# Kernel optimization log

Hardware: AMD Instinct MI355X
Metric: run time of the kernel (lower is better)

Reference implementation:

```python
import jax, jax.numpy as jnp
import numpy as np

N_NODES = 50000
NEG_SLOPE = 0.2


def setup_inputs() -> dict:
    key = jax.random.key(0)
    k1, k2, k3, k4 = jax.random.split(key, 4)
    N, E, F, H, C = 50000, 800000, 128, 4, 32
    x = jax.random.normal(k1, (N, F), dtype=jnp.float32)
    edge_index = jax.random.randint(k2, (2, E), 0, N, dtype=jnp.int32)
    weight = jax.random.normal(k3, (F, H * C), dtype=jnp.float32) * 0.1  # glorot-ish scale
    att = jax.random.normal(k4, (1, H, 2 * C), dtype=jnp.float32) * 0.1
    bias = jnp.zeros((C,), dtype=jnp.float32)
    return {"x": x, "edge_index": edge_index, "weight": weight, "att": att, "bias": bias}


def reference(x, edge_index, weight, att, bias):
    N = x.shape[0]
    H, C2 = att.shape[1], att.shape[2]
    C = C2 // 2
    # linear projection -> [N, H, C]
    xw = jnp.matmul(x, weight).reshape(N, H, C)
    row, col = edge_index[0], edge_index[1]
    # per-edge attention logits: gather both endpoints, concat along channel
    x_i = xw[row]                     # [E, H, C]
    x_j = xw[col]                     # [E, H, C]
    cat_x = jnp.concatenate([x_i, x_j], axis=-1)      # [E, H, 2C]
    alpha = jnp.sum(cat_x * att, axis=-1)             # [E, H]
    alpha = jnp.where(alpha >= 0, alpha, NEG_SLOPE * alpha)  # leaky_relu
    # segment softmax grouped by row (source index, as in the torch code)
    seg_max = jax.ops.segment_max(alpha, row, num_segments=N)
    seg_max = jnp.where(jnp.isfinite(seg_max), seg_max, 0.0)
    alpha = jnp.exp(alpha - seg_max[row])
    seg_sum = jax.ops.segment_sum(alpha, row, num_segments=N)
    alpha = alpha / (seg_sum[row] + 1e-16)            # [E, H]
    # PyG propagate: message = alpha * x_j where x_j = x[edge_index[0]],
    # aggregated (scatter-add) into target = edge_index[1]
    msg = alpha[..., None] * xw[row]                  # [E, H, C]
    out = jax.ops.segment_sum(msg, col, num_segments=N)  # [N, H, C]
    out = out.mean(axis=1) + bias                     # concat=False -> head mean, + bias
    return out
```

## Files before the change

### kernel.cpp

```cpp
#include <hip/hip_runtime.h>
#include <hip/hip_fp16.h>

#define FDIM 128
#define HEADS 4
#define CD 32
#define BM 64
#define XPAD 68

static __device__ __forceinline__ unsigned short f2bf(float v) {
    unsigned u = __float_as_uint(v);
    u += 0x7FFF + ((u >> 16) & 1);
    return (unsigned short)(u >> 16);
}
static __device__ __forceinline__ float bf2f(unsigned short u) {
    return __uint_as_float(((unsigned)u) << 16);
}

__global__ __launch_bounds__(256) void k_gemm(const float* __restrict__ x,
                                              const float* __restrict__ w,
                                              unsigned short* __restrict__ xwh,
                                              float4* __restrict__ zero_base,
                                              int nz4, int N)
{
    __shared__ float xs[FDIM * XPAD];
    int t = threadIdx.x;
    int row0 = blockIdx.x * BM;
    for (int i = blockIdx.x * 256 + t; i < nz4; i += gridDim.x * 256)
        zero_base[i] = make_float4(0.f, 0.f, 0.f, 0.f);
#pragma unroll
    for (int it = 0; it < 8; it++) {
        int i = t + 256 * it;
        int row = i & 63, kq = i >> 6;
        float4 v = make_float4(0.f, 0.f, 0.f, 0.f);
        if (row0 + row < N) v = ((const float4*)x)[(size_t)(row0 + row) * 32 + kq];
        xs[(kq * 4 + 0) * XPAD + row] = v.x;
        xs[(kq * 4 + 1) * XPAD + row] = v.y;
        xs[(kq * 4 + 2) * XPAD + row] = v.z;
        xs[(kq * 4 + 3) * XPAD + row] = v.w;
    }
    __syncthreads();
    int tx = t & 31, ty = t >> 5;
    int c0 = tx * 4, r0 = ty * 8;
    const float4* w4 = (const float4*)w;
    float acc[8][4];
#pragma unroll
    for (int i = 0; i < 8; i++)
#pragma unroll
        for (int j = 0; j < 4; j++) acc[i][j] = 0.f;
#pragma unroll 4
    for (int k = 0; k < FDIM; k++) {
        float4 wv = w4[k * 32 + tx];
        float4 xa = *(const float4*)&xs[k * XPAD + r0];
        float4 xb = *(const float4*)&xs[k * XPAD + r0 + 4];
        float xr[8] = {xa.x, xa.y, xa.z, xa.w, xb.x, xb.y, xb.z, xb.w};
        float wr[4] = {wv.x, wv.y, wv.z, wv.w};
#pragma unroll
        for (int i = 0; i < 8; i++)
#pragma unroll
            for (int j = 0; j < 4; j++) acc[i][j] += xr[i] * wr[j];
    }
    int h = c0 >> 5, chb = c0 & 31;
#pragma unroll
    for (int i = 0; i < 8; i++) {
        int r = row0 + r0 + i;
        if (r < N) {
#pragma unroll
            for (int j = 0; j < 4; j++)
                xwh[(size_t)r * FDIM + (chb + j) * 4 + h] = f2bf(acc[i][j]);
        }
    }
}

__global__ __launch_bounds__(256) void k_logits(const unsigned short* __restrict__ xwh,
                                                const float* __restrict__ att,
                                                float* __restrict__ a_src,
                                                float* __restrict__ a_dst, int N)
{
    __shared__ float attl[HEADS * 2 * CD];
    int t = threadIdx.x;
    attl[t] = att[t];
    __syncthreads();
    int n = blockIdx.x * 256 + t;
    if (n >= N) return;
    const ushort4* xp = (const ushort4*)(xwh + (size_t)n * FDIM);
    float s[4] = {0.f, 0.f, 0.f, 0.f}, d[4] = {0.f, 0.f, 0.f, 0.f};
#pragma unroll 8
    for (int c = 0; c < CD; c++) {
        ushort4 p = xp[c];
        float f0 = bf2f(p.x), f1 = bf2f(p.y), f2 = bf2f(p.z), f3 = bf2f(p.w);
        s[0] += f0 * attl[0 * 64 + c];  d[0] += f0 * attl[0 * 64 + 32 + c];
        s[1] += f1 * attl[1 * 64 + c];  d[1] += f1 * attl[1 * 64 + 32 + c];
        s[2] += f2 * attl[2 * 64 + c];  d[2] += f2 * attl[2 * 64 + 32 + c];
        s[3] += f3 * attl[3 * 64 + c];  d[3] += f3 * attl[3 * 64 + 32 + c];
    }
    *(float4*)&a_src[n * 4] = make_float4(s[0], s[1], s[2], s[3]);
    *(float4*)&a_dst[n * 4] = make_float4(d[0], d[1], d[2], d[3]);
}

__global__ __launch_bounds__(256) void k_esum(const int* __restrict__ ei, int E,
                                              const float* __restrict__ a_src,
                                              const float* __restrict__ a_dst,
                                              float* __restrict__ seg,
                                              float* __restrict__ ealpha)
{
    int gid = blockIdx.x * 256 + threadIdx.x;
    if (gid >= E * HEADS) return;
    int e = gid >> 2, h = gid & 3;
    int r = ei[e], cl = ei[E + e];
    float a = a_src[r * 4 + h] + a_dst[cl * 4 + h];
    a = a >= 0.f ? a : 0.2f * a;
    float ex = __expf(a);
    ealpha[gid] = ex;
    atomicAdd(&seg[r * 4 + h], ex);
}

__global__ __launch_bounds__(256) void k_scatter(const int* __restrict__ ei, int E,
                                                 const float* __restrict__ ealpha,
                                                 const float* __restrict__ seg,
                                                 const unsigned short* __restrict__ xwh,
                                                 __half2* __restrict__ out_acc2)
{
    int t = threadIdx.x;
    int le = t >> 4, c2 = t & 15;
    int e = blockIdx.x * 16 + le;
    if (e >= E) return;
    int r = ei[e], cl = ei[E + e];
    int lane = t & 63;
    float av = 0.f;
    if (c2 < 4) av = 0.25f * ealpha[e * 4 + c2] / (seg[r * 4 + c2] + 1e-16f);
    uint4 q = ((const uint4*)(xwh + (size_t)r * FDIM))[c2];
    float a0 = __shfl(av, (lane & 48) + 0, 64);
    float a1 = __shfl(av, (lane & 48) + 1, 64);
    float a2 = __shfl(av, (lane & 48) + 2, 64);
    float a3 = __shfl(av, (lane & 48) + 3, 64);
    float v0 = a0 * bf2f((unsigned short)(q.x & 0xFFFF)) + a1 * bf2f((unsigned short)(q.x >> 16))
             + a2 * bf2f((unsigned short)(q.y & 0xFFFF)) + a3 * bf2f((unsigned short)(q.y >> 16));
    float v1 = a0 * bf2f((unsigned short)(q.z & 0xFFFF)) + a1 * bf2f((unsigned short)(q.z >> 16))
             + a2 * bf2f((unsigned short)(q.w & 0xFFFF)) + a3 * bf2f((unsigned short)(q.w >> 16));
    unsafeAtomicAdd(&out_acc2[(size_t)cl * 16 + c2], __floats2half2_rn(v0, v1));
}

__global__ void k_final(const __half2* __restrict__ out_acc2, const float4* __restrict__ bias,
                        float4* __restrict__ out, int N)
{
    int i = blockIdx.x * 256 + threadIdx.x;
    if (i >= N * 8) return;
    float4 b = bias[i & 7];
    float2 f0 = __half22float2(out_acc2[i * 2]);
    float2 f1 = __half22float2(out_acc2[i * 2 + 1]);
    out[i] = make_float4(f0.x + b.x, f0.y + b.y, f1.x + b.z, f1.y + b.w);
}

extern "C" void kernel_launch(void* const* d_in, const int* in_sizes, int n_in,
                              void* d_out, int out_size, void* d_ws, size_t ws_size,
                              hipStream_t stream)
{
    const float* x    = (const float*)d_in[0];
    const int*   ei   = (const int*)d_in[1];
    const float* w    = (const float*)d_in[2];
    const float* att  = (const float*)d_in[3];
    const float* bias = (const float*)d_in[4];
    float* out = (float*)d_out;
    int N = in_sizes[0] / FDIM;
    int E = in_sizes[1] / 2;

    unsigned short* xwh = (unsigned short*)d_ws;
    float* fws      = (float*)(xwh + (size_t)N * FDIM);
    float* a_src    = fws;
    float* a_dst    = a_src + (size_t)N * HEADS;
    float* ealpha   = a_dst + (size_t)N * HEADS;
    float* seg      = ealpha + (size_t)E * HEADS;
    __half2* out_acc2 = (__half2*)(seg + (size_t)N * HEADS);

    int nz4 = (N * HEADS + N * CD / 2 + 3) / 4;

    k_gemm<<<(N + BM - 1) / BM, 256, 0, stream>>>(x, w, xwh, (float4*)seg, nz4, N);
    k_logits<<<(N + 255) / 256, 256, 0, stream>>>(xwh, att, a_src, a_dst, N);
    k_esum<<<(E * HEADS + 255) / 256, 256, 0, stream>>>(ei, E, a_src, a_dst, seg, ealpha);
    k_scatter<<<(E + 15) / 16, 256, 0, stream>>>(ei, E, ealpha, seg, xwh, out_acc2);
    k_final<<<(N * 8 + 255) / 256, 256, 0, stream>>>(out_acc2, (const float4*)bias, (float4*)out, N);
}
```

Baseline: 214.1 us.

## Fuse attention logit computation into GEMM epilogue and store edge exps as fp16

The separate logits kernel is removed. After the GEMM, each block stages its fp32 accumulators in shared memory and computes the per-node source and destination attention dot products there, which saves a kernel launch and a re-read of the bf16 projection. The per-edge exponentials are now stored as half precision instead of float, halving that intermediate buffer's traffic between the edge-sum and scatter kernels. The logits now use fp32 values instead of bf16-rounded ones, which changes numerics slightly. The fp16 exps could overflow for large logits.

```diff
diff --git a/kernel.cpp b/kernel.cpp
--- a/kernel.cpp
+++ b/kernel.cpp
@@ -18,15 +18,20 @@
 
 __global__ __launch_bounds__(256) void k_gemm(const float* __restrict__ x,
                                               const float* __restrict__ w,
+                                              const float* __restrict__ att,
                                               unsigned short* __restrict__ xwh,
+                                              float* __restrict__ a_src,
+                                              float* __restrict__ a_dst,
                                               float4* __restrict__ zero_base,
                                               int nz4, int N)
 {
     __shared__ float xs[FDIM * XPAD];
+    __shared__ float attl[HEADS * 2 * CD];
     int t = threadIdx.x;
     int row0 = blockIdx.x * BM;
     for (int i = blockIdx.x * 256 + t; i < nz4; i += gridDim.x * 256)
         zero_base[i] = make_float4(0.f, 0.f, 0.f, 0.f);
+    attl[t] = att[t];
 #pragma unroll
     for (int it = 0; it < 8; it++) {
         int i = t + 256 * it;
@@ -59,49 +64,38 @@
 #pragma unroll
             for (int j = 0; j < 4; j++) acc[i][j] += xr[i] * wr[j];
     }
-    int h = c0 >> 5, chb = c0 & 31;
+    int h0 = c0 >> 5, chb = c0 & 31;
 #pragma unroll
     for (int i = 0; i < 8; i++) {
         int r = row0 + r0 + i;
         if (r < N) {
 #pragma unroll
             for (int j = 0; j < 4; j++)
-                xwh[(size_t)r * FDIM + (chb + j) * 4 + h] = f2bf(acc[i][j]);
+                xwh[(size_t)r * FDIM + (chb + j) * 4 + h0] = f2bf(acc[i][j]);
         }
     }
-}
-
-__global__ __launch_bounds__(256) void k_logits(const unsigned short* __restrict__ xwh,
-                                                const float* __restrict__ att,
-                                                float* __restrict__ a_src,
-                                                float* __restrict__ a_dst, int N)
-{
-    __shared__ float attl[HEADS * 2 * CD];
-    int t = threadIdx.x;
-    attl[t] = att[t];
     __syncthreads();
-    int n = blockIdx.x * 256 + t;
-    if (n >= N) return;
-    const ushort4* xp = (const ushort4*)(xwh + (size_t)n * FDIM);
-    float s[4] = {0.f, 0.f, 0.f, 0.f}, d[4] = {0.f, 0.f, 0.f, 0.f};
+    float* accs = xs;
+#pragma unroll
+    for (int i = 0; i < 8; i++)
+        *(float4*)&accs[(r0 + i) * 132 + c0] =
+            make_float4(acc[i][0], acc[i][1], acc[i][2], acc[i][3]);
+    __syncthreads();
+    int row = t >> 2, h = t & 3;
+    const float* ap = &attl[h * 2 * CD];
+    const float* xr = &accs[row * 132 + h * CD];
+    float s = 0.f, d = 0.f;
 #pragma unroll 8
-    for (int c = 0; c < CD; c++) {
-        ushort4 p = xp[c];
-        float f0 = bf2f(p.x), f1 = bf2f(p.y), f2 = bf2f(p.z), f3 = bf2f(p.w);
-        s[0] += f0 * attl[0 * 64 + c];  d[0] += f0 * attl[0 * 64 + 32 + c];
-        s[1] += f1 * attl[1 * 64 + c];  d[1] += f1 * attl[1 * 64 + 32 + c];
-        s[2] += f2 * attl[2 * 64 + c];  d[2] += f2 * attl[2 * 64 + 32 + c];
-        s[3] += f3 * attl[3 * 64 + c];  d[3] += f3 * attl[3 * 64 + 32 + c];
-    }
-    *(float4*)&a_src[n * 4] = make_float4(s[0], s[1], s[2], s[3]);
-    *(float4*)&a_dst[n * 4] = make_float4(d[0], d[1], d[2], d[3]);
+    for (int c = 0; c < CD; c++) { float v = xr[c]; s += v * ap[c]; d += v * ap[CD + c]; }
+    int n = row0 + row;
+    if (n < N) { a_src[n * 4 + h] = s; a_dst[n * 4 + h] = d; }
 }
 
 __global__ __launch_bounds__(256) void k_esum(const int* __restrict__ ei, int E,
                                               const float* __restrict__ a_src,
                                               const float* __restrict__ a_dst,
                                               float* __restrict__ seg,
-                                              float* __restrict__ ealpha)
+                                              __half* __restrict__ ealpha)
 {
     int gid = blockIdx.x * 256 + threadIdx.x;
     if (gid >= E * HEADS) return;
@@ -110,12 +104,12 @@
     float a = a_src[r * 4 + h] + a_dst[cl * 4 + h];
     a = a >= 0.f ? a : 0.2f * a;
     float ex = __expf(a);
-    ealpha[gid] = ex;
+    ealpha[gid] = __float2half(ex);
     atomicAdd(&seg[r * 4 + h], ex);
 }
 
 __global__ __launch_bounds__(256) void k_scatter(const int* __restrict__ ei, int E,
-                                                 const float* __restrict__ ealpha,
+                                                 const __half* __restrict__ ealpha,
                                                  const float* __restrict__ seg,
                                                  const unsigned short* __restrict__ xwh,
                                                  __half2* __restrict__ out_acc2)
@@ -127,7 +121,7 @@
     int r = ei[e], cl = ei[E + e];
     int lane = t & 63;
     float av = 0.f;
-    if (c2 < 4) av = 0.25f * ealpha[e * 4 + c2] / (seg[r * 4 + c2] + 1e-16f);
+    if (c2 < 4) av = 0.25f * __half2float(ealpha[e * 4 + c2]) / (seg[r * 4 + c2] + 1e-16f);
     uint4 q = ((const uint4*)(xwh + (size_t)r * FDIM))[c2];
     float a0 = __shfl(av, (lane & 48) + 0, 64);
     float a1 = __shfl(av, (lane & 48) + 1, 64);
@@ -168,14 +162,14 @@
     float* fws      = (float*)(xwh + (size_t)N * FDIM);
     float* a_src    = fws;
     float* a_dst    = a_src + (size_t)N * HEADS;
-    float* ealpha   = a_dst + (size_t)N * HEADS;
-    float* seg      = ealpha + (size_t)E * HEADS;
+    float* seg      = a_dst + (size_t)N * HEADS;
     __half2* out_acc2 = (__half2*)(seg + (size_t)N * HEADS);
+    __half* ealpha  = (__half*)(out_acc2 + (size_t)N * 16);
 
-    int nz4 = (N * HEADS + N * CD / 2 + 3) / 4;
+    int nz4 = N * 5;
 
-    k_gemm<<<(N + BM - 1) / BM, 256, 0, stream>>>(x, w, xwh, (float4*)seg, nz4, N);
-    k_logits<<<(N + 255) / 256, 256, 0, stream>>>(xwh, att, a_src, a_dst, N);
+    k_gemm<<<(N + BM - 1) / BM, 256, 0, stream>>>(x, w, att, xwh, a_src, a_dst,
+                                                  (float4*)seg, nz4, N);
     k_esum<<<(E * HEADS + 255) / 256, 256, 0, stream>>>(ei, E, a_src, a_dst, seg, ealpha);
     k_scatter<<<(E + 15) / 16, 256, 0, stream>>>(ei, E, ealpha, seg, xwh, out_acc2);
     k_final<<<(N * 8 + 255) / 256, 256, 0, stream>>>(out_acc2, (const float4*)bias, (float4*)out, N);
```

New measurement: 210.2 us. No clear change (-1.8%).
